# Performance work log

Hardware: AMD Instinct MI355X
Metric: run time of the kernel (lower is better)

The kernel has to match this reference:

```python
import jax, jax.numpy as jnp
import numpy as np

D_MODEL = 1024
NUM_HEADS = 16
D_HEAD = 64  # d_q = d_k = d_v
BATCH = 4
SEQ = 2048


def _trunc_normal(key, shape, std):
    # truncated normal in [-3*std, 3*std], matching nn.init.trunc_normal_
    return jax.random.truncated_normal(key, -3.0, 3.0, shape, dtype=jnp.float32) * std


def setup_inputs() -> dict:
    key = jax.random.key(0)
    k_x, k_q, k_k, k_v, k_o = jax.random.split(key, 5)
    hd = NUM_HEADS * D_HEAD
    s_in = np.sqrt(2.0 / (D_MODEL + hd))
    s_out = np.sqrt(2.0 / (hd + D_MODEL))
    return {
        "in_features": jax.random.normal(k_x, (BATCH, SEQ, D_MODEL), dtype=jnp.float32),
        "w_q": _trunc_normal(k_q, (hd, D_MODEL), s_in),
        "w_k": _trunc_normal(k_k, (hd, D_MODEL), s_in),
        "w_v": _trunc_normal(k_v, (hd, D_MODEL), s_in),
        "w_o": _trunc_normal(k_o, (D_MODEL, hd), s_out),
    }


def reference(in_features, w_q, w_k, w_v, w_o):
    B, S, D = in_features.shape
    H, Dh = NUM_HEADS, D_HEAD
    # QKV projections (weight stored as [out, in])
    q = jnp.einsum('od,bsd->bso', w_q, in_features).reshape(B, S, H, Dh).transpose(0, 2, 1, 3)
    k = jnp.einsum('od,bsd->bso', w_k, in_features).reshape(B, S, H, Dh).transpose(0, 2, 1, 3)
    v = jnp.einsum('od,bsd->bso', w_v, in_features).reshape(B, S, H, Dh).transpose(0, 2, 1, 3)
    # scaled dot-product attention with dense causal mask (as in source)
    att = jnp.einsum('bhqd,bhkd->bhqk', q, k) / jnp.sqrt(jnp.float32(Dh)).astype(q.dtype)
    causal = jnp.tril(jnp.ones((S, S), dtype=bool))
    att = jnp.where(causal, att, -jnp.inf)
    att = jax.nn.softmax(att, axis=-1)
    out = jnp.einsum('bhqk,bhkd->bhqd', att, v)  # [B,H,S,Dh]
    out = out.transpose(0, 2, 1, 3).reshape(B, S, H * Dh)
    return jnp.einsum('od,bsd->bso', w_o, out)
```

## Files before the change

kernel.cpp:

```cpp
#include <hip/hip_runtime.h>
#include <stdint.h>

#define D_MODEL 1024
#define NHEADS  16
#define DHEAD   64
#define BATCH   4
#define SEQ     2048
#define MTOT    (BATCH*SEQ)

typedef unsigned short u16;
typedef uint32_t u32;
typedef __bf16 bf16x8 __attribute__((ext_vector_type(8)));
typedef float  f32x4  __attribute__((ext_vector_type(4)));
typedef float  f32x16 __attribute__((ext_vector_type(16)));
typedef u16    u16x8  __attribute__((ext_vector_type(8)));
typedef u16    u16x4  __attribute__((ext_vector_type(4)));
typedef u32    u32x4  __attribute__((ext_vector_type(4)));

__device__ __forceinline__ u16 f2bf(float f) {
  uint32_t u = __builtin_bit_cast(uint32_t, f);
  u += 0x7fff + ((u >> 16) & 1);
  return (u16)(u >> 16);
}

__device__ __forceinline__ void gll16(const u16* g, u16* lds) {
  __builtin_amdgcn_global_load_lds(
      (__attribute__((address_space(1))) void*)(g),
      (__attribute__((address_space(3))) void*)(lds), 16, 0, 0);
}

__global__ void cvtk(const float4* __restrict__ in, u16x4* __restrict__ out, int n4) {
  const int i = blockIdx.x * blockDim.x + threadIdx.x;
  if (i < n4) {
    const float4 f = in[i];
    u16x4 h;
    h[0] = f2bf(f.x); h[1] = f2bf(f.y); h[2] = f2bf(f.z); h[3] = f2bf(f.w);
    out[i] = h;
  }
}

__global__ void cvtk4(const float4* __restrict__ a, const float4* __restrict__ b,
                      const float4* __restrict__ c, const float4* __restrict__ d,
                      u16x4* __restrict__ out, int n4) {
  const int i = blockIdx.x * blockDim.x + threadIdx.x;
  if (i >= n4) return;
  const float4* src = (blockIdx.y == 0) ? a : (blockIdx.y == 1) ? b
                    : (blockIdx.y == 2) ? c : d;
  const float4 f = src[i];
  u16x4 h;
  h[0] = f2bf(f.x); h[1] = f2bf(f.y); h[2] = f2bf(f.z); h[3] = f2bf(f.w);
  out[(size_t)blockIdx.y * n4 + i] = h;
}

#define QSLOT 16384

__global__ __launch_bounds__(512, 2) void gemm_qkv8(
    const u16* __restrict__ A, const u16* __restrict__ Bw, u16* __restrict__ Out)
{
  extern __shared__ u16 qsm[];
  const int tid = threadIdx.x;
  const int w = tid >> 6, l = tid & 63;
  const int wm = w >> 2, wn = w & 3;
  const int bid = blockIdx.x;
  const int wg = (bid & 7) * 48 + (bid >> 3);
  const int m0 = (wg / 12) * 256, n0 = (wg % 12) * 256;

  const int srow = l >> 2;
  const int sc   = (l & 3) ^ ((l >> 3) & 3);
  const int nA0 = w * 2, nA1 = w * 2 + 1;
  const u16* gA0 = A  + (size_t)(m0 + nA0*16 + srow) * 1024 + sc*8;
  const u16* gA1 = A  + (size_t)(m0 + nA1*16 + srow) * 1024 + sc*8;
  const u16* gB0 = Bw + (size_t)(n0 + nA0*16 + srow) * 1024 + sc*8;
  const u16* gB1 = Bw + (size_t)(n0 + nA1*16 + srow) * 1024 + sc*8;

  const int cp = ((l >> 4) ^ ((l >> 1) & 3)) * 8;
  const int ra = wm * 128 + (l & 15);
  const int rb = wn * 64 + (l & 15);

  f32x4 acc[8][4];
  #pragma unroll
  for (int i = 0; i < 8; ++i)
    #pragma unroll
    for (int j = 0; j < 4; ++j)
      acc[i][j] = f32x4{0.f, 0.f, 0.f, 0.f};

#define QSTAGE(slot, s) do {                                          \
    gll16(gA0 + (s)*32, qsm + (slot)*QSLOT + nA0*512);                \
    gll16(gA1 + (s)*32, qsm + (slot)*QSLOT + nA1*512);                \
    gll16(gB0 + (s)*32, qsm + (slot)*QSLOT + 8192 + nA0*512);         \
    gll16(gB1 + (s)*32, qsm + (slot)*QSLOT + 8192 + nA1*512);         \
  } while (0)

#define QCOMP(slot) do {                                                        \
    const u16* As_ = qsm + (slot)*QSLOT;                                        \
    const u16* Bs_ = As_ + 8192;                                                \
    bf16x8 af[8], bfr[4];                                                       \
    _Pragma("unroll")                                                           \
    for (int mf = 0; mf < 8; ++mf)                                              \
      af[mf] = *(const bf16x8*)&As_[(ra + mf*16)*32 + cp];                      \
    _Pragma("unroll")                                                           \
    for (int nf = 0; nf < 4; ++nf)                                              \
      bfr[nf] = *(const bf16x8*)&Bs_[(rb + nf*16)*32 + cp];                     \
    __builtin_amdgcn_s_setprio(1);                                              \
    _Pragma("unroll")                                                           \
    for (int mf = 0; mf < 8; ++mf)                                              \
      _Pragma("unroll")                                                         \
      for (int nf = 0; nf < 4; ++nf)                                            \
        acc[mf][nf] = __builtin_amdgcn_mfma_f32_16x16x32_bf16(af[mf], bfr[nf],  \
                                                              acc[mf][nf], 0, 0, 0); \
    __builtin_amdgcn_s_setprio(0);                                              \
  } while (0)

  QSTAGE(0, 0);
  QSTAGE(1, 1);
  asm volatile("s_waitcnt vmcnt(4)" ::: "memory");
  __builtin_amdgcn_s_barrier();
  __builtin_amdgcn_sched_barrier(0);

  #pragma unroll 2
  for (int s = 0; s < 30; ++s) {
    QSTAGE((s + 2) & 3, s + 2);
    QCOMP(s & 3);
    asm volatile("s_waitcnt vmcnt(4)" ::: "memory");
    __builtin_amdgcn_s_barrier();
    __builtin_amdgcn_sched_barrier(0);
  }
  QCOMP(2);
  asm volatile("s_waitcnt vmcnt(0)" ::: "memory");
  __builtin_amdgcn_s_barrier();
  __builtin_amdgcn_sched_barrier(0);
  QCOMP(3);

#undef QSTAGE
#undef QCOMP

  const float scale = (n0 < 1024) ? 0.125f * 1.44269504088896f : 1.0f;
  const int g = l >> 4, c15 = l & 15;
  #pragma unroll
  for (int mf = 0; mf < 8; ++mf) {
    #pragma unroll
    for (int nf = 0; nf < 4; ++nf) {
      #pragma unroll
      for (int j = 0; j < 4; ++j) {
        const int row = m0 + wm*128 + mf*16 + g*4 + j;
        const int col = n0 + wn*64 + nf*16 + c15;
        const int z = col >> 10;
        const int wi = col & 1023;
        const int b = row >> 11, sq = row & (SEQ-1);
        const int h = wi >> 6, dh = wi & (DHEAD-1);
        Out[(size_t)z * MTOT * D_MODEL
            + ((size_t)(b*NHEADS + h) * SEQ + sq) * DHEAD + dh] =
            f2bf(acc[mf][nf][j] * scale);
      }
    }
  }
}

template<int MODE>
__launch_bounds__(256)
__global__ void gemm_bt_k(const u16* __restrict__ A,
                          const u16* __restrict__ W0,
                          const u16* __restrict__ W1,
                          const u16* __restrict__ W2,
                          void* __restrict__ Cout)
{
  constexpr int K = D_MODEL;
  const int tid = threadIdx.x;
  const int l = tid & 63, w = tid >> 6;
  const int m0 = blockIdx.x * 128;
  const int n0 = blockIdx.y * 128;
  const u16* Bm = W0;

  __shared__ __align__(16) u16 As[128*32];
  __shared__ __align__(16) u16 Bs[128*32];

  f32x4 acc[4][4];
  #pragma unroll
  for (int i = 0; i < 4; ++i)
    #pragma unroll
    for (int j = 0; j < 4; ++j)
      acc[i][j] = f32x4{0.f, 0.f, 0.f, 0.f};

  const int wr = w >> 1, wc = w & 1;
  const int srow = l >> 2;
  const int scol = (l & 3) * 8;

  for (int k0 = 0; k0 < K; k0 += 32) {
    __syncthreads();
    #pragma unroll
    for (int j = 0; j < 2; ++j) {
      const int seg = w * 2 + j;
      gll16(A  + (size_t)(m0 + seg*16 + srow) * K + k0 + scol, &As[seg*512]);
      gll16(Bm + (size_t)(n0 + seg*16 + srow) * K + k0 + scol, &Bs[seg*512]);
    }
    __syncthreads();
    bf16x8 af[4], bfr[4];
    #pragma unroll
    for (int m = 0; m < 4; ++m)
      af[m] = *(const bf16x8*)&As[(wr*64 + m*16 + (l & 15))*32 + (l >> 4)*8];
    #pragma unroll
    for (int n = 0; n < 4; ++n)
      bfr[n] = *(const bf16x8*)&Bs[(wc*64 + n*16 + (l & 15))*32 + (l >> 4)*8];
    #pragma unroll
    for (int m = 0; m < 4; ++m)
      #pragma unroll
      for (int n = 0; n < 4; ++n)
        acc[m][n] = __builtin_amdgcn_mfma_f32_16x16x32_bf16(af[m], bfr[n], acc[m][n], 0, 0, 0);
  }

  const int g = l >> 4, c15 = l & 15;
  #pragma unroll
  for (int m = 0; m < 4; ++m) {
    #pragma unroll
    for (int n = 0; n < 4; ++n) {
      #pragma unroll
      for (int j = 0; j < 4; ++j) {
        const int row = m0 + wr*64 + m*16 + g*4 + j;
        const int col = n0 + wc*64 + n*16 + c15;
        ((float*)Cout)[(size_t)row * D_MODEL + col] = acc[m][n][j];
      }
    }
  }
}

__launch_bounds__(512, 2)
__global__ void attn6_k(const u16* __restrict__ Qb, const u16* __restrict__ Kb_,
                        const u16* __restrict__ Vb_, u16* __restrict__ Oa)
{
  const int tid = threadIdx.x;
  const int w = tid >> 6, l = tid & 63;
  const int q5 = l & 31, hi = l >> 5;
  const int r = blockIdx.x;
  const int bh = (r & 7) * 8 + ((r >> 3) & 7);
  const int pairi = r >> 6;
  const int b = bh >> 4, h = bh & 15;
  const size_t base = (size_t)bh * SEQ * DHEAD;
  const u16* Qg = Qb + base;
  const u16* Kg = Kb_ + base;
  const u16* Vg = Vb_ + base;

  __shared__ __align__(16) u16 smem[32768];

  const int kc = tid & 7, rp = tid >> 3;
  const int vsub = rp >> 5;
  const int rp5 = rp & 31;
  int vIdx32[8];
  #pragma unroll
  for (int e = 0; e < 8; ++e)
    vIdx32[e] = vsub*2048 + (8*kc + e)*32 + ((((rp5 >> 2) ^ kc ^ e) & 7) << 2) + (rp5 & 3);

  const int kr8 = l >> 3;
  const int kkv = 8*w + kr8;
  const int kdc = (l & 7) ^ kr8 ^ w;

  for (int half = 0; half < 2; ++half) {
    const int tq = half ? (7 - pairi) : pairi;
    const int q0w = tq*256 + 32*w;
    const int ntk = (tq + 1) * 2;
    const int ntw = (q0w >> 7) + 1;

    bf16x8 qf[4];
    #pragma unroll
    for (int s = 0; s < 4; ++s)
      qf[s] = *(const bf16x8*)(Qg + (size_t)(q0w + q5)*DHEAD + 16*s + 8*hi);

    f32x16 c0 = {}, c1 = {};
    float mrun = -1e30f, lrun = 0.f;

    {
      #pragma unroll
      for (int h2 = 0; h2 < 2; ++h2)
        gll16(Kg + (size_t)(64*h2 + kkv)*DHEAD + kdc*8, smem + h2*4096 + w*512);
      const u16x8 v0 = *(const u16x8*)(Vg + (size_t)(2*rp)*DHEAD + kc*8);
      const u16x8 v1 = *(const u16x8*)(Vg + (size_t)(2*rp + 1)*DHEAD + kc*8);
      u32* Vd = (u32*)(smem + 16384);
      #pragma unroll
      for (int e = 0; e < 8; ++e)
        Vd[vIdx32[e]] = (u32)v0[e] | ((u32)v1[e] << 16);
    }
    __syncthreads();

    for (int t = 0; t < ntk; ++t) {
      const int cur = t & 1;
      const bool pf = (t + 1 < ntk);
      u16x8 v0, v1;
      if (pf) {
        const int kv1 = (t + 1) * 128;
        v0 = *(const u16x8*)(Vg + (size_t)(kv1 + 2*rp)*DHEAD + kc*8);
        v1 = *(const u16x8*)(Vg + (size_t)(kv1 + 2*rp + 1)*DHEAD + kc*8);
        #pragma unroll
        for (int h2 = 0; h2 < 2; ++h2)
          gll16(Kg + (size_t)(kv1 + 64*h2 + kkv)*DHEAD + kdc*8,
                smem + (cur^1)*8192 + h2*4096 + w*512);
      }

      if (t < ntw) {
        const u16* Kb = smem + cur*8192;
        const u16* Vv = smem + 16384 + cur*8192;

        f32x16 st[4] = {{}, {}, {}, {}};
        __builtin_amdgcn_s_setprio(1);
        #pragma unroll
        for (int kbg = 0; kbg < 4; ++kbg) {
          #pragma unroll
          for (int s = 0; s < 4; ++s) {
            const int slot = ((2*s + hi) ^ (l & 7) ^ ((4*(kbg & 1)) & 7) ^ (q5 >> 3)) & 7;
            const bf16x8 kf = *(const bf16x8*)(Kb + (kbg >> 1)*4096
                                               + ((kbg & 1)*32 + q5)*64 + slot*8);
            st[kbg] = __builtin_amdgcn_mfma_f32_32x32x16_bf16(kf, qf[s], st[kbg], 0, 0, 0);
          }
        }
        __builtin_amdgcn_s_setprio(0);

        if (t == ntw - 1) {
          const int kv0 = t * 128;
          #pragma unroll
          for (int kbg = 0; kbg < 4; ++kbg)
            #pragma unroll
            for (int rr = 0; rr < 16; ++rr) {
              const int kvg = kv0 + 32*kbg + (rr & 3) + 8*(rr >> 2) + 4*hi;
              if (kvg > q0w + q5) st[kbg][rr] = -1e30f;
            }
        }

        float mx = -1e30f;
        #pragma unroll
        for (int kbg = 0; kbg < 4; ++kbg)
          #pragma unroll
          for (int rr = 0; rr < 16; ++rr) mx = fmaxf(mx, st[kbg][rr]);
        mx = fmaxf(mx, __shfl_xor(mx, 32));
        float alpha = 1.0f;
        if (!__all(mx <= mrun + 8.0f)) {
          const float mnew = fmaxf(mrun, mx);
          alpha = __builtin_amdgcn_exp2f(mrun - mnew);
          mrun = mnew;
          #pragma unroll
          for (int rr = 0; rr < 16; ++rr) { c0[rr] *= alpha; c1[rr] *= alpha; }
        }
        float rs = 0.f;
        #pragma unroll
        for (int kbg = 0; kbg < 4; ++kbg)
          #pragma unroll
          for (int rr = 0; rr < 16; ++rr) {
            const float pe = __builtin_amdgcn_exp2f(st[kbg][rr] - mrun);
            st[kbg][rr] = pe;
            rs += pe;
          }
        rs += __shfl_xor(rs, 32);
        lrun = lrun * alpha + rs;

        bf16x8 pb[8];
        #pragma unroll
        for (int kbg = 0; kbg < 4; ++kbg) {
          u32 pw[8];
          #pragma unroll
          for (int i = 0; i < 8; ++i) {
            u32 t0;
            asm("v_cvt_pk_bf16_f32 %0, %1, %2"
                : "=v"(t0) : "v"(st[kbg][2*i]), "v"(st[kbg][2*i+1]));
            pw[i] = t0;
          }
          asm("v_permlane32_swap_b32 %0, %1" : "+v"(pw[0]), "+v"(pw[2]));
          asm("v_permlane32_swap_b32 %0, %1" : "+v"(pw[1]), "+v"(pw[3]));
          asm("v_permlane32_swap_b32 %0, %1" : "+v"(pw[4]), "+v"(pw[6]));
          asm("v_permlane32_swap_b32 %0, %1" : "+v"(pw[5]), "+v"(pw[7]));
          pb[2*kbg]   = __builtin_bit_cast(bf16x8, u32x4{pw[0], pw[1], pw[2], pw[3]});
          pb[2*kbg+1] = __builtin_bit_cast(bf16x8, u32x4{pw[4], pw[5], pw[6], pw[7]});
        }

        __builtin_amdgcn_s_setprio(1);
        #pragma unroll
        for (int h2 = 0; h2 < 2; ++h2) {
          #pragma unroll
          for (int s = 0; s < 4; ++s) {
            {
              const int slot = ((2*s + hi) ^ (l & 7) ^ (q5 >> 3)) & 7;
              const bf16x8 vf = *(const bf16x8*)(Vv + h2*4096 + q5*64 + slot*8);
              c0 = __builtin_amdgcn_mfma_f32_32x32x16_bf16(vf, pb[4*h2 + s], c0, 0, 0, 0);
            }
            {
              const int slot = ((2*s + hi) ^ (l & 7) ^ 4 ^ (q5 >> 3)) & 7;
              const bf16x8 vf = *(const bf16x8*)(Vv + h2*4096 + (32 + q5)*64 + slot*8);
              c1 = __builtin_amdgcn_mfma_f32_32x32x16_bf16(vf, pb[4*h2 + s], c1, 0, 0, 0);
            }
          }
        }
        __builtin_amdgcn_s_setprio(0);
      }

      if (pf) {
        u32* Vd = (u32*)(smem + 16384) + (cur^1)*4096;
        #pragma unroll
        for (int e = 0; e < 8; ++e)
          Vd[vIdx32[e]] = (u32)v0[e] | ((u32)v1[e] << 16);
      }
      __syncthreads();
    }

    const float linv = __builtin_amdgcn_rcpf(lrun);
    #pragma unroll
    for (int Ab = 0; Ab < 2; ++Ab)
      #pragma unroll
      for (int rr = 0; rr < 16; ++rr) {
        const int d = 32*Ab + (rr & 3) + 8*(rr >> 2) + 4*hi;
        smem[w*2048 + q5*64 + (((d >> 3) ^ (q5 & 7)) & 7)*8 + (d & 7)] =
            f2bf((Ab ? c1[rr] : c0[rr]) * linv);
      }
    __syncthreads();
    #pragma unroll
    for (int cc = 0; cc < 4; ++cc) {
      const int dchunk = 4*hi + cc;
      const u16x8 vv = *(const u16x8*)&smem[w*2048 + q5*64 + ((dchunk ^ (q5 & 7)) & 7)*8];
      *(u16x8*)(Oa + (size_t)(b*SEQ + q0w + q5)*D_MODEL + h*DHEAD + 32*hi + 8*cc) = vv;
    }
    __syncthreads();
  }
}

extern "C" void kernel_launch(void* const* d_in, const int* in_sizes, int n_in,
                              void* d_out, int out_size, void* d_ws, size_t ws_size,
                              hipStream_t stream) {
  const float* X  = (const float*)d_in[0];
  const float* Wq = (const float*)d_in[1];
  const float* Wk = (const float*)d_in[2];
  const float* Wv = (const float*)d_in[3];
  const float* Wo = (const float*)d_in[4];

  u16* xb  = (u16*)d_ws;
  u16* wqb = xb  + (size_t)MTOT*D_MODEL;
  u16* wkb = wqb + (size_t)D_MODEL*D_MODEL;
  u16* wvb = wkb + (size_t)D_MODEL*D_MODEL;
  u16* wob = wvb + (size_t)D_MODEL*D_MODEL;
  u16* qkv = wob + (size_t)D_MODEL*D_MODEL;
  u16* att = qkv + (size_t)3*MTOT*D_MODEL;

  (void)hipFuncSetAttribute((const void*)gemm_qkv8,
                            hipFuncAttributeMaxDynamicSharedMemorySize, 131072);

  const int nx4 = MTOT*D_MODEL/4;
  const int nw4 = D_MODEL*D_MODEL/4;
  cvtk<<<nx4/256, 256, 0, stream>>>((const float4*)X, (u16x4*)xb, nx4);
  dim3 gc(nw4/256, 4, 1);
  cvtk4<<<gc, 256, 0, stream>>>((const float4*)Wq, (const float4*)Wk,
                                (const float4*)Wv, (const float4*)Wo,
                                (u16x4*)wqb, nw4);

  gemm_qkv8<<<384, 512, 131072, stream>>>(xb, wqb, qkv);

  attn6_k<<<256, 512, 0, stream>>>(qkv, qkv + (size_t)MTOT*D_MODEL,
                                   qkv + (size_t)2*MTOT*D_MODEL, att);

  dim3 g3(MTOT/128, D_MODEL/128, 1);
  gemm_bt_k<0><<<g3, 256, 0, stream>>>(att, wob, nullptr, nullptr, d_out);
}
```

Measured before the change: 162.2 us.

## Restructure QKV GEMM into ping-pong K=64 stages with interleaved loads and MFMA phases

Rewrites the fused QKV projection GEMM main loop to use K-tiles of 64 instead of 32, split into eight 128x64 shared-memory slots arranged as two ping-pong buffers. Each iteration interleaves global-to-LDS loads for future tiles with four MFMA sub-phases, separated by barriers, and uses a new 8-way XOR swizzle. The aim is to halve loop iterations and hide load latency behind matrix work. The cost is many more barriers per iteration and a more fragile hand-written schedule.

```diff
diff --git a/kernel.cpp b/kernel.cpp
--- a/kernel.cpp
+++ b/kernel.cpp
@@ -52,9 +52,47 @@
   out[(size_t)blockIdx.y * n4 + i] = h;
 }
 
-#define QSLOT 16384
-
-__global__ __launch_bounds__(512, 2) void gemm_qkv8(
+#define QS 8192
+
+#define BARS() __builtin_amdgcn_s_barrier()
+#define LGKM0() do { asm volatile("s_waitcnt lgkmcnt(0)" ::: "memory"); \
+                     __builtin_amdgcn_sched_barrier(0); } while (0)
+
+#define STG(pbase, roff, t_, slot_) do {                                        \
+    gll16((pbase) + (size_t)(roff)*1024 + (t_)*64,      qsm + (slot_)*QS + w*512);        \
+    gll16((pbase) + (size_t)((roff)+64)*1024 + (t_)*64, qsm + (slot_)*QS + w*512 + 4096); \
+  } while (0)
+
+#define PH_READS_A() do {                                                       \
+    _Pragma("unroll")                                                           \
+    for (int mf = 0; mf < 8; ++mf) {                                            \
+      af0[mf] = *(const bf16x8*)&sA[(mf*16 + r15)*64 + cs0];                    \
+      af1[mf] = *(const bf16x8*)&sA[(mf*16 + r15)*64 + cs1];                    \
+    }                                                                           \
+    _Pragma("unroll")                                                           \
+    for (int nf = 0; nf < 4; ++nf)                                              \
+      bq[nf] = *(const bf16x8*)&sB[(brow + nf*16 + r15)*64 + cs0];              \
+  } while (0)
+
+#define PH_READS_B1() do {                                                      \
+    _Pragma("unroll")                                                           \
+    for (int nf = 0; nf < 4; ++nf)                                              \
+      bq[nf] = *(const bf16x8*)&sB[(brow + nf*16 + r15)*64 + cs1];              \
+  } while (0)
+
+#define MM(AF, N0, N1) do {                                                     \
+    __builtin_amdgcn_s_setprio(1);                                              \
+    _Pragma("unroll")                                                           \
+    for (int mf = 0; mf < 8; ++mf) {                                            \
+      acc[mf][N0] = __builtin_amdgcn_mfma_f32_16x16x32_bf16(AF[mf], bq[N0],     \
+                                                            acc[mf][N0], 0,0,0);\
+      acc[mf][N1] = __builtin_amdgcn_mfma_f32_16x16x32_bf16(AF[mf], bq[N1],     \
+                                                            acc[mf][N1], 0,0,0);\
+    }                                                                           \
+    __builtin_amdgcn_s_setprio(0);                                              \
+  } while (0)
+
+__global__ __launch_bounds__(512, 2) void gemm_qkv8p(
     const u16* __restrict__ A, const u16* __restrict__ Bw, u16* __restrict__ Out)
 {
   extern __shared__ u16 qsm[];
@@ -65,17 +103,15 @@
   const int wg = (bid & 7) * 48 + (bid >> 3);
   const int m0 = (wg / 12) * 256, n0 = (wg % 12) * 256;
 
-  const int srow = l >> 2;
-  const int sc   = (l & 3) ^ ((l >> 3) & 3);
-  const int nA0 = w * 2, nA1 = w * 2 + 1;
-  const u16* gA0 = A  + (size_t)(m0 + nA0*16 + srow) * 1024 + sc*8;
-  const u16* gA1 = A  + (size_t)(m0 + nA1*16 + srow) * 1024 + sc*8;
-  const u16* gB0 = Bw + (size_t)(n0 + nA0*16 + srow) * 1024 + sc*8;
-  const u16* gB1 = Bw + (size_t)(n0 + nA1*16 + srow) * 1024 + sc*8;
-
-  const int cp = ((l >> 4) ^ ((l >> 1) & 3)) * 8;
-  const int ra = wm * 128 + (l & 15);
-  const int rb = wn * 64 + (l & 15);
+  const int sr  = 8*w + (l >> 3);
+  const int sc8 = ((l & 7) ^ ((l >> 3) & 7)) * 8;
+  const u16* pA = A  + (size_t)(m0 + sr) * 1024 + sc8;
+  const u16* pB = Bw + (size_t)(n0 + sr) * 1024 + sc8;
+
+  const int r15 = l & 15;
+  const int cs0 = (((l >> 4) + 0) ^ (l & 7)) * 8;
+  const int cs1 = (((l >> 4) + 4) ^ (l & 7)) * 8;
+  const int brow = (wn & 1) * 64;
 
   f32x4 acc[8][4];
   #pragma unroll
@@ -84,55 +120,77 @@
     for (int j = 0; j < 4; ++j)
       acc[i][j] = f32x4{0.f, 0.f, 0.f, 0.f};
 
-#define QSTAGE(slot, s) do {                                          \
-    gll16(gA0 + (s)*32, qsm + (slot)*QSLOT + nA0*512);                \
-    gll16(gA1 + (s)*32, qsm + (slot)*QSLOT + nA1*512);                \
-    gll16(gB0 + (s)*32, qsm + (slot)*QSLOT + 8192 + nA0*512);         \
-    gll16(gB1 + (s)*32, qsm + (slot)*QSLOT + 8192 + nA1*512);         \
-  } while (0)
-
-#define QCOMP(slot) do {                                                        \
-    const u16* As_ = qsm + (slot)*QSLOT;                                        \
-    const u16* Bs_ = As_ + 8192;                                                \
-    bf16x8 af[8], bfr[4];                                                       \
-    _Pragma("unroll")                                                           \
-    for (int mf = 0; mf < 8; ++mf)                                              \
-      af[mf] = *(const bf16x8*)&As_[(ra + mf*16)*32 + cp];                      \
-    _Pragma("unroll")                                                           \
-    for (int nf = 0; nf < 4; ++nf)                                              \
-      bfr[nf] = *(const bf16x8*)&Bs_[(rb + nf*16)*32 + cp];                     \
-    __builtin_amdgcn_s_setprio(1);                                              \
-    _Pragma("unroll")                                                           \
-    for (int mf = 0; mf < 8; ++mf)                                              \
-      _Pragma("unroll")                                                         \
-      for (int nf = 0; nf < 4; ++nf)                                            \
-        acc[mf][nf] = __builtin_amdgcn_mfma_f32_16x16x32_bf16(af[mf], bfr[nf],  \
-                                                              acc[mf][nf], 0, 0, 0); \
-    __builtin_amdgcn_s_setprio(0);                                              \
-  } while (0)
-
-  QSTAGE(0, 0);
-  QSTAGE(1, 1);
-  asm volatile("s_waitcnt vmcnt(4)" ::: "memory");
-  __builtin_amdgcn_s_barrier();
+  STG(pA, 0,   0, 0);
+  STG(pA, 128, 0, 1);
+  STG(pB, 0,   0, 2);
+  STG(pB, 128, 0, 3);
+  STG(pA, 0,   1, 4);
+  STG(pA, 128, 1, 5);
+  STG(pB, 0,   1, 6);
+  asm volatile("s_waitcnt vmcnt(6)" ::: "memory");
+  BARS();
   __builtin_amdgcn_sched_barrier(0);
 
   #pragma unroll 2
-  for (int s = 0; s < 30; ++s) {
-    QSTAGE((s + 2) & 3, s + 2);
-    QCOMP(s & 3);
-    asm volatile("s_waitcnt vmcnt(4)" ::: "memory");
-    __builtin_amdgcn_s_barrier();
+  for (int t = 0; t < 14; ++t) {
+    const int p = t & 1, po = p ^ 1;
+    const u16* sA = qsm + (size_t)(p*4 + wm) * QS;
+    const u16* sB = qsm + (size_t)(p*4 + 2 + (wn >> 1)) * QS;
+    bf16x8 af0[8], af1[8], bq[4];
+    PH_READS_A();
+    STG(pB, 128, t+1, po*4 + 3);
+    BARS(); LGKM0();
+    MM(af0, 0, 1);
+    BARS();
+    STG(pA, 0, t+2, p*4 + 0);
+    BARS();
+    MM(af0, 2, 3);
+    BARS();
+    PH_READS_B1();
+    STG(pA, 128, t+2, p*4 + 1);
+    BARS(); LGKM0();
+    MM(af1, 0, 1);
+    BARS();
+    STG(pB, 0, t+2, p*4 + 2);
+    BARS();
+    MM(af1, 2, 3);
+    asm volatile("s_waitcnt vmcnt(6)" ::: "memory");
+    BARS();
     __builtin_amdgcn_sched_barrier(0);
   }
-  QCOMP(2);
-  asm volatile("s_waitcnt vmcnt(0)" ::: "memory");
-  __builtin_amdgcn_s_barrier();
-  __builtin_amdgcn_sched_barrier(0);
-  QCOMP(3);
-
-#undef QSTAGE
-#undef QCOMP
+
+  {
+    const u16* sA = qsm + (size_t)(0*4 + wm) * QS;
+    const u16* sB = qsm + (size_t)(0*4 + 2 + (wn >> 1)) * QS;
+    bf16x8 af0[8], af1[8], bq[4];
+    PH_READS_A();
+    STG(pB, 128, 15, 4 + 3);
+    BARS(); LGKM0();
+    MM(af0, 0, 1);
+    BARS();
+    BARS();
+    MM(af0, 2, 3);
+    BARS();
+    PH_READS_B1();
+    BARS(); LGKM0();
+    MM(af1, 0, 1);
+    BARS();
+    MM(af1, 2, 3);
+    asm volatile("s_waitcnt vmcnt(0)" ::: "memory");
+    BARS();
+    __builtin_amdgcn_sched_barrier(0);
+  }
+  {
+    const u16* sA = qsm + (size_t)(1*4 + wm) * QS;
+    const u16* sB = qsm + (size_t)(1*4 + 2 + (wn >> 1)) * QS;
+    bf16x8 af0[8], af1[8], bq[4];
+    PH_READS_A();
+    MM(af0, 0, 1);
+    MM(af0, 2, 3);
+    PH_READS_B1();
+    MM(af1, 0, 1);
+    MM(af1, 2, 3);
+  }
 
   const float scale = (n0 < 1024) ? 0.125f * 1.44269504088896f : 1.0f;
   const int g = l >> 4, c15 = l & 15;
@@ -155,6 +213,11 @@
     }
   }
 }
+
+#undef STG
+#undef PH_READS_A
+#undef PH_READS_B1
+#undef MM
 
 template<int MODE>
 __launch_bounds__(256)
@@ -434,7 +497,7 @@
   u16* qkv = wob + (size_t)D_MODEL*D_MODEL;
   u16* att = qkv + (size_t)3*MTOT*D_MODEL;
 
-  (void)hipFuncSetAttribute((const void*)gemm_qkv8,
+  (void)hipFuncSetAttribute((const void*)gemm_qkv8p,
                             hipFuncAttributeMaxDynamicSharedMemorySize, 131072);
 
   const int nx4 = MTOT*D_MODEL/4;
@@ -445,7 +508,7 @@
                                 (const float4*)Wv, (const float4*)Wo,
                                 (u16x4*)wqb, nw4);
 
-  gemm_qkv8<<<384, 512, 131072, stream>>>(xb, wqb, qkv);
+  gemm_qkv8p<<<384, 512, 131072, stream>>>(xb, wqb, qkv);
 
   attn6_k<<<256, 512, 0, stream>>>(qkv, qkv + (size_t)MTOT*D_MODEL,
                                    qkv + (size_t)2*MTOT*D_MODEL, att);
```

After: 160.8 us. Within noise of the previous version (-0.8%).
